# Kernel tuning notes

Hardware: AMD Instinct MI355X
Metric: run time of the kernel (lower is better)

The kernel has to match this reference:

```python
import jax, jax.numpy as jnp
import numpy as np
from jax.scipy.special import logsumexp

BN_EPS = 1e-5
K_CLUSTERS = 32


def _conv1x1(x, W, b):
    # x: [B, Cin, N], W: [Cout, Cin] -> [B, Cout, N]
    return jnp.einsum('oc,bcn->bon', W, x) + b[None, :, None]


def _bn3(x, g, b):
    # BatchNorm1d (training mode, batch stats) over [B, C, N]
    m = x.mean(axis=(0, 2), keepdims=True)
    v = x.var(axis=(0, 2), keepdims=True)
    return g[None, :, None] * (x - m) / jnp.sqrt(v + BN_EPS) + b[None, :, None]


def _bn2(x, g, b):
    # BatchNorm1d (training mode, batch stats) over [B, C]
    m = x.mean(axis=0)
    v = x.var(axis=0)
    return g * (x - m) / jnp.sqrt(v + BN_EPS) + b


def _conv_proj(x, w1, b1, g1, t1, w2, b2, g2, t2, w3, b3):
    h = jax.nn.relu(_bn3(_conv1x1(x, w1, b1), g1, t1))
    h = jax.nn.relu(_bn3(_conv1x1(h, w2, b2), g2, t2))
    return _conv1x1(h, w3, b3)


def _mlp_proj(x, w1, b1, g1, t1, w2, b2, g2, t2, w3, b3):
    h = jax.nn.relu(_bn2(x @ w1.T + b1, g1, t1))
    h = jax.nn.relu(_bn2(h @ w2.T + b2, g2, t2))
    return h @ w3.T + b3


def _normalize(x, axis):
    n = jnp.linalg.norm(x, axis=axis, keepdims=True)
    return x / jnp.maximum(n, 1e-12)


def _sinkhorn_gamma(cost, p, q, eps=1e-3, thresh=1e-3, max_iter=25):
    # log-domain Sinkhorn with early stopping, mirrors the torch loop exactly
    logp = jnp.log(p + 1e-8)
    logq = jnp.log(q + 1e-8)

    def Kf(u, v):
        return (-cost + u[..., :, None] + v[..., None, :]) / eps

    def body(st):
        i, u, v, _ = st
        u0, v0 = u, v
        u = eps * (logp - logsumexp(Kf(u, v), axis=-1)) + u
        v = eps * (logq - logsumexp(Kf(u, v), axis=-2)) + v
        d = jnp.mean(jnp.sum(jnp.abs(u - u0), -1) + jnp.sum(jnp.abs(v - v0), -1))
        return i + 1, u, v, d

    def cond(st):
        return (st[0] < max_iter) & (st[3] >= thresh)

    init = (0, jnp.zeros_like(p), jnp.zeros_like(q), jnp.asarray(jnp.inf, cost.dtype))
    _, u, v, _ = jax.lax.while_loop(cond, body, init)
    return jnp.exp(Kf(u, v))


def _forward(features,
             cw1, cb1, cg1, ct1, cw2, cb2, cg2, ct2, cw3, cb3,
             pw1, pb1, pg1, pt1, pw2, pb2, pg2, pt2, pw3, pb3,
             mw1, mb1, mg1, mt1, mw2, mb2, mg2, mt2, mw3, mb3):
    bs, dim, num = features.shape
    Kc = K_CLUSTERS

    log_score = _conv_proj(features, cw1, cb1, cg1, ct1, cw2, cb2, cg2, ct2, cw3, cb3)  # [B,K,N]
    score = jax.nn.softmax(log_score, axis=1)
    pi = jax.lax.stop_gradient(jnp.clip(score.sum(-1), 1e-4)[:, None, :])  # [B,1,K]
    vlad = jnp.einsum('bkn,bdn->bdk', score, features) / pi  # [B,D,K] (mu == vlad)

    # no-grad Sinkhorn assignment (xyz is None branch, dst='fe')
    nf = _normalize(jax.lax.stop_gradient(features), axis=1)
    nmu = _normalize(jax.lax.stop_gradient(vlad), axis=1)
    cost = jax.lax.stop_gradient(2.0 - 2.0 * jnp.einsum('bdn,bdm->bnm', nf, nmu))  # [B,N,K]
    p = jnp.full((bs, num), 1.0 / num, dtype=features.dtype)
    q = jnp.full((bs, Kc), 1.0 / Kc, dtype=features.dtype)
    gamma = _sinkhorn_gamma(cost, p, q, eps=1e-3, thresh=1e-3, max_iter=25)
    assign = jax.lax.stop_gradient(num * jnp.swapaxes(gamma, -1, -2))  # [B,K,N]

    loss = -jnp.mean(jnp.sum(assign * jax.nn.log_softmax(log_score, axis=1), axis=1))

    c_vlad = _mlp_proj(jnp.max(vlad, axis=-1),
                       mw1, mb1, mg1, mt1, mw2, mb2, mg2, mt2, mw3, mb3)  # [B,proj]
    vlad_out = _conv_proj(vlad, pw1, pb1, pg1, pt1, pw2, pb2, pg2, pt2, pw3, pb3)  # [B,proj,K]
    return loss, vlad_out, c_vlad


def setup_inputs() -> dict:
    B, D, N, Kc, H, P = 8, 1024, 4096, 32, 512, 128
    key = jax.random.key(0)
    ks = jax.random.split(key, 16)

    def w(k, out_c, in_c):
        return (jax.random.normal(k, (out_c, in_c), jnp.float32) / np.sqrt(in_c)).astype(jnp.float32)

    d = {'features': jax.random.normal(ks[0], (B, D, N), jnp.float32)}
    # score conv head: D -> H -> H -> Kc  (hidden = dim // 2 = 512)
    d.update(cw1=w(ks[1], H, D), cb1=jnp.zeros(H), cg1=jnp.ones(H), ct1=jnp.zeros(H),
             cw2=w(ks[2], H, H), cb2=jnp.zeros(H), cg2=jnp.ones(H), ct2=jnp.zeros(H),
             cw3=w(ks[3], Kc, H), cb3=jnp.zeros(Kc))
    # projector conv: D -> 512 -> 512 -> P
    d.update(pw1=w(ks[4], H, D), pb1=jnp.zeros(H), pg1=jnp.ones(H), pt1=jnp.zeros(H),
             pw2=w(ks[5], H, H), pb2=jnp.zeros(H), pg2=jnp.ones(H), pt2=jnp.zeros(H),
             pw3=w(ks[6], P, H), pb3=jnp.zeros(P))
    # predictor MLP: D -> 512 -> 512 -> P
    d.update(mw1=w(ks[7], H, D), mb1=jnp.zeros(H), mg1=jnp.ones(H), mt1=jnp.zeros(H),
             mw2=w(ks[8], H, H), mb2=jnp.zeros(H), mg2=jnp.ones(H), mt2=jnp.zeros(H),
             mw3=w(ks[9], P, H), mb3=jnp.zeros(P))
    return d


def reference(features,
              cw1, cb1, cg1, ct1, cw2, cb2, cg2, ct2, cw3, cb3,
              pw1, pb1, pg1, pt1, pw2, pb2, pg2, pt2, pw3, pb3,
              mw1, mb1, mg1, mt1, mw2, mb2, mg2, mt2, mw3, mb3):
    return _forward(features,
                    cw1, cb1, cg1, ct1, cw2, cb2, cg2, ct2, cw3, cb3,
                    pw1, pb1, pg1, pt1, pw2, pb2, pg2, pt2, pw3, pb3,
                    mw1, mb1, mg1, mt1, mw2, mb2, mg2, mt2, mw3, mb3)
```

## Files before the change

### kernel.cpp

```cpp
#include <hip/hip_runtime.h>
#include <cmath>

#define BB 8
#define DD 1024
#define NP 4096
#define KC 32
#define HH 512
#define PP 128
#define NJB 16
#define BN_EPS 1e-5f
#define NSLOT 32

typedef unsigned short u16;
typedef unsigned long long u64;
typedef short s16x8 __attribute__((ext_vector_type(8)));
typedef float f32x4 __attribute__((ext_vector_type(4)));

__device__ __forceinline__ float waveReduceSum(float v) {
#pragma unroll
  for (int o = 32; o > 0; o >>= 1) v += __shfl_down(v, o, 64);
  return v;
}

__device__ __forceinline__ void split3(float y, short& h, short& m, short& l) {
  unsigned uy = __float_as_uint(y);
  h = (short)(uy >> 16);
  float r1 = y - __uint_as_float(uy & 0xFFFF0000u);
  unsigned um = __float_as_uint(r1);
  m = (short)(um >> 16);
  float r2 = r1 - __uint_as_float(um & 0xFFFF0000u);
  l = (short)(__float_as_uint(r2) >> 16);
}

__global__ __launch_bounds__(256) void convW3_all(
    const float* __restrict__ W1, u16* __restrict__ h1, u16* __restrict__ m1, u16* __restrict__ l1,
    const float* __restrict__ W2, u16* __restrict__ h2, u16* __restrict__ m2, u16* __restrict__ l2,
    const float* __restrict__ W3, u16* __restrict__ h3, u16* __restrict__ m3, u16* __restrict__ l3,
    float* __restrict__ zbuf) {
  int z = blockIdx.z;
  if (z == 2 && blockIdx.x >= 1) {
    int id = (blockIdx.x - 1) * 32 + blockIdx.y;
#pragma unroll
    for (int k2 = 0; k2 < 3; k2++) {
      int idx = k2 * 24576 + id * 256 + (int)threadIdx.x;
      if (idx < 69632) zbuf[idx] = 0.f;
    }
    return;
  }
  const float* W; u16 *hb, *mb, *lb; int K, BM, MTt, KCH;
  if (z == 0)      { W = W1; hb = h1; mb = m1; lb = l1; K = 1024; BM = 128; MTt = 4; KCH = 32; }
  else if (z == 1) { W = W2; hb = h2; mb = m2; lb = l2; K = 512;  BM = 128; MTt = 4; KCH = 16; }
  else             { W = W3; hb = h3; mb = m3; lb = l3; K = 512;  BM = 32;  MTt = 1; KCH = 16; }
  int mt = blockIdx.x, kc = blockIdx.y;
  if (mt >= MTt || kc >= KCH) return;
  const int AU = BM * 4;
  for (int u = threadIdx.x; u < AU; u += 256) {
    int q = u / BM, m = u % BM;
    const float* wp = W + (size_t)(mt * BM + m) * K + kc * 32 + q * 8;
    s16x8 hv, mv, lv;
#pragma unroll
    for (int j = 0; j < 8; j++) {
      short h, mm, l; split3(wp[j], h, mm, l);
      hv[j] = h; mv[j] = mm; lv[j] = l;
    }
    size_t ob = ((size_t)(mt * KCH + kc)) * (size_t)(BM * 32) + (size_t)u * 8;
    *(s16x8*)(hb + ob) = hv;
    *(s16x8*)(mb + ob) = mv;
    *(s16x8*)(lb + ob) = lv;
  }
}

template<int BM, int MBLK, int MT, int NT, int WM, bool BNRELU, bool ACCST, bool SMAX>
__global__ __launch_bounds__(256) void gemm_mfma3(
    const u16* __restrict__ wh, const u16* __restrict__ wmid, const u16* __restrict__ wl,
    const float* __restrict__ bias, const float* __restrict__ X,
    const float* __restrict__ insum, const float* __restrict__ insq,
    const float* __restrict__ bng, const float* __restrict__ bnb, float cnt,
    float* __restrict__ Y, int K, int M,
    float* __restrict__ gsum, float* __restrict__ gsq,
    float* __restrict__ score, float* __restrict__ lse, float* __restrict__ piraw) {
  __shared__ s16x8 AhS[BM * 4], AmS[BM * 4], AlS[BM * 4];
  __shared__ s16x8 BhS[512], BmS[512], BlS[512];
  __shared__ float scS[512], shS[512];
  const int KCH = K / 32;
  const int tid = threadIdx.x;
  const int bz = blockIdx.z;
  int bid = blockIdx.x;
  int xs = bid & 7, rr = bid >> 3;
  int m_idx = rr % MBLK;
  int n_idx = xs + 8 * (rr / MBLK);

  const int w = tid >> 6, l = tid & 63, q = l >> 4, col = l & 15;
  const int wm = (WM == 1) ? 0 : (w >> 1);
  const int wn = (WM == 1) ? w : (w & 1);
  constexpr int NA = (BM * 4 + 255) / 256;

  if (BNRELU) {
    for (int c0 = tid; c0 < K; c0 += 256) {
      float s = 0.f, q2 = 0.f;
      for (int sl = 0; sl < NSLOT; sl++) { s += insum[sl * 512 + c0]; q2 += insq[sl * 512 + c0]; }
      float mean = s / cnt;
      float var = q2 / cnt - mean * mean;
      float sc = bng[c0] / sqrtf(var + BN_EPS);
      scS[c0] = sc; shS[c0] = bnb[c0] - mean * sc;
    }
    __syncthreads();
  }

  f32x4 acc[MT][NT];
#pragma unroll
  for (int i = 0; i < MT; i++)
#pragma unroll
    for (int j = 0; j < NT; j++) { acc[i][j][0] = 0.f; acc[i][j][1] = 0.f; acc[i][j][2] = 0.f; acc[i][j][3] = 0.f; }

// ... 231 lines not shown
      float ra[8], rb[2];
#pragma unroll
      for (int i = 0; i < 8; i++) ra[i] = As[kk][ty * 8 + i];
      rb[0] = Bs[kk][tx * 2]; rb[1] = Bs[kk][tx * 2 + 1];
#pragma unroll
      for (int i = 0; i < 8; i++) { acc[i][0] = fmaf(ra[i], rb[0], acc[i][0]); acc[i][1] = fmaf(ra[i], rb[1], acc[i][1]); }
    }
    __syncthreads();
  }
#pragma unroll
  for (int i = 0; i < 8; i++)
#pragma unroll
    for (int j = 0; j < 2; j++)
      atomicAdd(&vlad[((size_t)b * DD + d0 + ty * 8 + i) * KC + tx * 2 + j], acc[i][j]);
}

__global__ __launch_bounds__(256) void cost_accum(
    const float* __restrict__ feat, const float* __restrict__ vlad,
    const float* __restrict__ piraw, float* __restrict__ costd,
    float* __restrict__ nfsq, float* __restrict__ nmusq, float* __restrict__ gmax) {
  int sp = blockIdx.x, nt = blockIdx.y, b = blockIdx.z;
  int n0 = nt * 128;
  int d_start = sp * (DD / 4);
  __shared__ float As[32][132];
  __shared__ float Bs[32][36];
  __shared__ float nfs[128];
  __shared__ float piS[KC];
  __shared__ float nms[KC];
  int tid = threadIdx.x;
  int tx = tid % 16;
  int ty = tid / 16;
  if (tid < KC) { piS[tid] = fmaxf(piraw[b * KC + tid], 1e-4f); nms[tid] = 0.f; }
  __syncthreads();
  float acc[8][2] = {};
  float sq = 0.f, nm_local = 0.f;
  const float* fb = feat + (size_t)b * DD * NP;
  const float* vb = vlad + (size_t)b * DD * KC;
  for (int dc = 0; dc < DD / 4; dc += 32) {
    int dd0 = d_start + dc;
    for (int i = tid; i < 32 * 128; i += 256) {
      int r = i >> 7, c = i & 127;
      float v = fb[(size_t)(dd0 + r) * NP + n0 + c];
      As[r][c] = v;
      sq = fmaf(v, v, sq);
    }
    for (int i = tid; i < 32 * 32; i += 256) {
      int r = i >> 5, c = i & 31;
      float v = vb[(size_t)(dd0 + r) * KC + c] / piS[c];
      Bs[r][c] = v;
      if (nt == 0) nm_local = fmaf(v, v, nm_local);
    }
    __syncthreads();
    if (nt == 0 && tid < 32) {
      float gm = -1e30f;
#pragma unroll
      for (int c = 0; c < KC; c++) gm = fmaxf(gm, Bs[tid][c]);
      gmax[(size_t)b * DD + dd0 + tid] = gm;
    }
#pragma unroll 4
    for (int kk = 0; kk < 32; kk++) {
      float ra[8], rb[2];
#pragma unroll
      for (int i = 0; i < 8; i++) ra[i] = As[kk][ty * 8 + i];
      rb[0] = Bs[kk][tx * 2]; rb[1] = Bs[kk][tx * 2 + 1];
#pragma unroll
      for (int i = 0; i < 8; i++) { acc[i][0] = fmaf(ra[i], rb[0], acc[i][0]); acc[i][1] = fmaf(ra[i], rb[1], acc[i][1]); }
    }
    __syncthreads();
  }
#pragma unroll
  for (int i = 0; i < 8; i++)
#pragma unroll
    for (int j = 0; j < 2; j++)
      atomicAdd(&costd[((size_t)b * NP + n0 + ty * 8 + i) * KC + tx * 2 + j], acc[i][j]);
  if (tid < 128) nfs[tid] = 0.f;
  __syncthreads();
  atomicAdd(&nfs[tid & 127], sq);
  if (nt == 0) atomicAdd(&nms[tid & 31], nm_local);
  __syncthreads();
  if (tid < 128) atomicAdd(&nfsq[(size_t)b * NP + n0 + tid], nfs[tid]);
  if (nt == 0 && tid < KC) atomicAdd(&nmusq[b * KC + tid], nms[tid]);
}

__global__ __launch_bounds__(256) void sinkhorn_all(
    const float* __restrict__ costd, const float* __restrict__ nfsq,
    const float* __restrict__ nmusq, u64* __restrict__ G,
    const float* __restrict__ LSm, const float* __restrict__ lseArr,
    float* __restrict__ out0, unsigned* __restrict__ flags,
    float logp, float logq) {
  const float EPS = 1e-3f, IEPS = 1000.f;
  int b = blockIdx.x / NJB, j = blockIdx.x % NJB;
  int tid = threadIdx.x;
  int n = j * 256 + tid;
  __shared__ float vsh[KC];
  __shared__ float nmS[KC];
  __shared__ float vals[256][33];
  __shared__ float red[KC][9];
  __shared__ float bmS[KC];
  __shared__ float redL[4];

  if (tid < KC) nmS[tid] = fmaxf(sqrtf(nmusq[b * KC + tid]), 1e-12f);
  __syncthreads();

  float c[KC];
  {
    const float* dp = costd + ((size_t)b * NP + n) * KC;
    float nf = fmaxf(sqrtf(nfsq[(size_t)b * NP + n]), 1e-12f);
#pragma unroll
    for (int k = 0; k < KC; k++) c[k] = 2.f - 2.f * dp[k] / (nf * nmS[k]);
  }

  const int kk = tid & 31, seg = tid >> 5;
  const int r0 = seg * 32;
  float u = 0.f;

  for (int t = 1; t <= 25; t++) {
    if (t > 1) {
      if (tid < NJB) {
        const unsigned* fp = flags + ((size_t)(t - 2) * BB + b) * NJB;
        while (__hip_atomic_load(&fp[tid], __ATOMIC_RELAXED, __HIP_MEMORY_SCOPE_AGENT) == 0u)
          __builtin_amdgcn_s_sleep(1);
      }
      __syncthreads();
    }
    if (tid < KC) {
      float v = 0.f;
      if (t > 1) {
        const u64* Gp = G + (((size_t)(t - 2) * BB + b) * NJB) * KC;
        float gm[NJB], gs[NJB];
#pragma unroll
        for (int jj = 0; jj < NJB; jj++) {
          u64 raw = __hip_atomic_load(&Gp[jj * KC + tid], __ATOMIC_RELAXED, __HIP_MEMORY_SCOPE_AGENT);
          gm[jj] = __uint_as_float((unsigned)raw);
          gs[jj] = __uint_as_float((unsigned)(raw >> 32));
        }
        float m = -1e30f;
#pragma unroll
        for (int jj = 0; jj < NJB; jj++) m = fmaxf(m, gm[jj]);
        float s = 0.f;
#pragma unroll
        for (int jj = 0; jj < NJB; jj++) s += gs[jj] * expf(gm[jj] - m);
        v = EPS * logq - EPS * (m + logf(s));
      }
      vsh[tid] = v;
    }
    __syncthreads();
    float m = -1e30f;
#pragma unroll
    for (int k = 0; k < KC; k++) m = fmaxf(m, vsh[k] - c[k]);
    float s = 0.f;
#pragma unroll
    for (int k = 0; k < KC; k++) s += expf((vsh[k] - c[k] - m) * IEPS);
    u = EPS * logp - m - EPS * logf(s);
#pragma unroll
    for (int k = 0; k < KC; k++) vals[tid][k] = (u - c[k]) * IEPS;
    __syncthreads();
    {
      float lm = -1e30f;
      for (int r = 0; r < 32; r++) lm = fmaxf(lm, vals[r0 + r][kk]);
      red[kk][seg] = lm;
    }
    __syncthreads();
    if (tid < KC) {
      float bm = red[tid][0];
      for (int i2 = 1; i2 < 8; i2++) bm = fmaxf(bm, red[tid][i2]);
      bmS[tid] = bm;
    }
    __syncthreads();
    {
      float bm = bmS[kk];
      float ls = 0.f;
      for (int r = 0; r < 32; r++) ls += expf(vals[r0 + r][kk] - bm);
      red[kk][seg] = ls;
    }
    __syncthreads();
    if (tid < KC) {
      float s8 = 0.f;
      for (int i2 = 0; i2 < 8; i2++) s8 += red[tid][i2];
      u64 raw = (u64)__float_as_uint(bmS[tid]) | ((u64)__float_as_uint(s8) << 32);
      u64* Gp = G + (((size_t)(t - 1) * BB + b) * NJB + j) * KC + tid;
      __hip_atomic_store(Gp, raw, __ATOMIC_RELAXED, __HIP_MEMORY_SCOPE_AGENT);
    }
    __syncthreads();
    if (tid == 0) {
      unsigned* fl = flags + ((size_t)(t - 1) * BB + b) * NJB + j;
      __hip_atomic_store(fl, 1u, __ATOMIC_RELAXED, __HIP_MEMORY_SCOPE_AGENT);
    }
  }

  if (tid < NJB) {
    const unsigned* fp = flags + ((size_t)24 * BB + b) * NJB;
    while (__hip_atomic_load(&fp[tid], __ATOMIC_RELAXED, __HIP_MEMORY_SCOPE_AGENT) == 0u)
      __builtin_amdgcn_s_sleep(1);
  }
  __syncthreads();
  __shared__ float v25S[KC];
  if (tid < KC) {
    const u64* Gp = G + (((size_t)24 * BB + b) * NJB) * KC;
    float gm[NJB], gs[NJB];
#pragma unroll
    for (int jj = 0; jj < NJB; jj++) {
      u64 raw = __hip_atomic_load(&Gp[jj * KC + tid], __ATOMIC_RELAXED, __HIP_MEMORY_SCOPE_AGENT);
      gm[jj] = __uint_as_float((unsigned)raw);
      gs[jj] = __uint_as_float((unsigned)(raw >> 32));
    }
    float m = -1e30f;
#pragma unroll
    for (int jj = 0; jj < NJB; jj++) m = fmaxf(m, gm[jj]);
    float s = 0.f;
#pragma unroll
    for (int jj = 0; jj < NJB; jj++) s += gs[jj] * expf(gm[jj] - m);
    v25S[tid] = EPS * logq - EPS * (m + logf(s));
  }
  __syncthreads();
  float lsev = lseArr[(size_t)b * NP + n];
  float part = 0.f;
#pragma unroll
  for (int k = 0; k < KC; k++) {
    float gamma = expf((u + v25S[k] - c[k]) * IEPS);
    float logsm = LSm[((size_t)b * KC + k) * NP + n] - lsev;
    part += gamma * logsm;
  }
  part *= (float)NP;
  int lane = tid & 63, wid = tid >> 6;
  part = waveReduceSum(part);
  if (lane == 0) redL[wid] = part;
  __syncthreads();
  if (tid == 0) {
    float tt = redL[0] + redL[1] + redL[2] + redL[3];
    atomicAdd(out0, -tt / (float)(BB * NP));
  }
}

template<int BM, int BN, int BK, int TM, int TN, bool BNRELU, bool ACCST, bool PDIV>
__global__ __launch_bounds__(256) void gemm_conv(
    const float* __restrict__ W, const float* __restrict__ bias,
    const float* __restrict__ X, float* __restrict__ Y,
    const float* __restrict__ pidiv,
    const float* __restrict__ insum, const float* __restrict__ insq,
    const float* __restrict__ bng, const float* __restrict__ bnb, float cnt,
    float* __restrict__ gsum, float* __restrict__ gsq,
    int M, int K, int N) {
  __shared__ float As[BK][BM + 4];
  __shared__ float Xs[BK][BN + 4];
  __shared__ float scS[512], shS[512];
  __shared__ float piS[BN + 4];
  const int b = blockIdx.z;
  const int m0 = blockIdx.y * BM;
  const int n0 = blockIdx.x * BN;
  const int tid = threadIdx.x;
  const int tx = tid % (BN / TN);
  const int ty = tid / (BN / TN);
  if (PDIV) {
    if (tid < N) piS[tid] = fmaxf(pidiv[b * N + tid], 1e-4f);
  }
  if (BNRELU) {
    for (int c0 = tid; c0 < K; c0 += 256) {
      float mean = insum[c0] / cnt;
      float var = insq[c0] / cnt - mean * mean;
      float sc = bng[c0] / sqrtf(var + BN_EPS);
      scS[c0] = sc; shS[c0] = bnb[c0] - mean * sc;
    }
  }
  if (PDIV || BNRELU) __syncthreads();
  const float* Xb = X + (size_t)b * K * N;
  float acc[TM][TN];
#pragma unroll
  for (int i = 0; i < TM; i++)
#pragma unroll
    for (int j = 0; j < TN; j++) acc[i][j] = 0.f;

  for (int k0 = 0; k0 < K; k0 += BK) {
    for (int i = tid; i < BM * BK; i += 256) {
      int r = i / BK, c = i % BK;
      As[c][r] = W[(size_t)(m0 + r) * K + k0 + c];
    }
    for (int i = tid; i < BK * BN; i += 256) {
      int r = i / BN, c = i % BN;
      float x = Xb[(size_t)(k0 + r) * N + n0 + c];
      if (PDIV) x /= piS[n0 + c];
      if (BNRELU) x = fmaxf(fmaf(x, scS[k0 + r], shS[k0 + r]), 0.f);
      Xs[r][c] = x;
    }
    __syncthreads();
#pragma unroll 4
    for (int kk = 0; kk < BK; kk++) {
      float ra[TM], rb[TN];
#pragma unroll
      for (int i = 0; i < TM; i++) ra[i] = As[kk][ty * TM + i];
#pragma unroll
      for (int j = 0; j < TN; j++) rb[j] = Xs[kk][tx * TN + j];
#pragma unroll
      for (int i = 0; i < TM; i++)
#pragma unroll
        for (int j = 0; j < TN; j++) acc[i][j] = fmaf(ra[i], rb[j], acc[i][j]);
    }
    __syncthreads();
  }
  float* red = (float*)As;
  if (ACCST) {
    if (tid < 2 * BM) red[tid] = 0.f;
    __syncthreads();
  }
#pragma unroll
  for (int i = 0; i < TM; i++) {
    int ml = ty * TM + i;
    float bm = bias[m0 + ml];
    float ys = 0.f, yq = 0.f;
#pragma unroll
    for (int j = 0; j < TN; j++) {
      float y = acc[i][j] + bm;
      Y[((size_t)b * M + m0 + ml) * N + n0 + tx * TN + j] = y;
      ys += y; yq = fmaf(y, y, yq);
    }
    if (ACCST) {
      atomicAdd(&red[ml * 2], ys);
      atomicAdd(&red[ml * 2 + 1], yq);
    }
  }
  if (ACCST) {
    __syncthreads();
    if (tid < BM) {
      atomicAdd(&gsum[m0 + tid], red[tid * 2]);
      atomicAdd(&gsq[m0 + tid], red[tid * 2 + 1]);
    }
  }
}

template<bool BNRELU, bool ACCST>
__global__ __launch_bounds__(256) void mlp_gemm(
    const float* __restrict__ W, const float* __restrict__ bias,
    const float* __restrict__ in, float* __restrict__ out,
    const float* __restrict__ insum, const float* __restrict__ insq,
    const float* __restrict__ g, const float* __restrict__ beta,
    float* __restrict__ gsum, float* __restrict__ gsq, int M, int K) {
  __shared__ float scS[512], shS[512];
  int tid = threadIdx.x;
  if (BNRELU) {
    for (int c0 = tid; c0 < K; c0 += 256) {
      float mean = insum[c0] * 0.125f;
      float var = insq[c0] * 0.125f - mean * mean;
      float sc = g[c0] / sqrtf(var + BN_EPS);
      scS[c0] = sc; shS[c0] = beta[c0] - mean * sc;
    }
    __syncthreads();
  }
  int gw = (blockIdx.x * 256 + tid) >> 6;
  int lane = tid & 63;
  int s = gw / M, jj = gw % M;
  const float4* ip = (const float4*)(in + (size_t)s * K);
  const float4* wp = (const float4*)(W + (size_t)jj * K);
  float acc = 0.f;
  for (int c4 = lane; c4 < (K >> 2); c4 += 64) {
    float4 x = ip[c4];
    float4 w = wp[c4];
    if (BNRELU) {
      int cb = c4 * 4;
      x.x = fmaxf(fmaf(x.x, scS[cb + 0], shS[cb + 0]), 0.f);
      x.y = fmaxf(fmaf(x.y, scS[cb + 1], shS[cb + 1]), 0.f);
      x.z = fmaxf(fmaf(x.z, scS[cb + 2], shS[cb + 2]), 0.f);
      x.w = fmaxf(fmaf(x.w, scS[cb + 3], shS[cb + 3]), 0.f);
    }
    acc += x.x * w.x + x.y * w.y + x.z * w.z + x.w * w.w;
  }
  acc = waveReduceSum(acc);
  if (lane == 0) {
    float y = acc + bias[jj];
    out[gw] = y;
    if (ACCST) { atomicAdd(&gsum[jj], y); atomicAdd(&gsq[jj], y * y); }
  }
}

extern "C" void kernel_launch(void* const* d_in, const int* in_sizes, int n_in,
                              void* d_out, int out_size, void* d_ws, size_t ws_size,
                              hipStream_t stream) {
  const float* feat = (const float*)d_in[0];
  const float* cw1 = (const float*)d_in[1];  const float* cb1 = (const float*)d_in[2];
  const float* cg1 = (const float*)d_in[3];  const float* ct1 = (const float*)d_in[4];
  const float* cw2 = (const float*)d_in[5];  const float* cb2 = (const float*)d_in[6];
  const float* cg2 = (const float*)d_in[7];  const float* ct2 = (const float*)d_in[8];
  const float* cw3 = (const float*)d_in[9];  const float* cb3 = (const float*)d_in[10];
  const float* pw1 = (const float*)d_in[11]; const float* pb1 = (const float*)d_in[12];
  const float* pg1 = (const float*)d_in[13]; const float* pt1 = (const float*)d_in[14];
  const float* pw2 = (const float*)d_in[15]; const float* pb2 = (const float*)d_in[16];
  const float* pg2 = (const float*)d_in[17]; const float* pt2 = (const float*)d_in[18];
  const float* pw3 = (const float*)d_in[19]; const float* pb3 = (const float*)d_in[20];
  const float* mw1 = (const float*)d_in[21]; const float* mb1 = (const float*)d_in[22];
  const float* mg1 = (const float*)d_in[23]; const float* mt1 = (const float*)d_in[24];
  const float* mw2 = (const float*)d_in[25]; const float* mb2 = (const float*)d_in[26];
  const float* mg2 = (const float*)d_in[27]; const float* mt2 = (const float*)d_in[28];
  const float* mw3 = (const float*)d_in[29]; const float* mb3 = (const float*)d_in[30];
  float* out = (float*)d_out;

  char* p = (char*)d_ws;
  size_t off = 0;
  auto alloc = [&](size_t bytes) { char* r = p + off; off = (off + bytes + 255) & ~(size_t)255; return r; };
  float* Y1 = (float*)alloc(67108864);
  float* Y2 = (float*)alloc(67108864);
  u16* W1H = (u16*)alloc(1048576); u16* W1M = (u16*)alloc(1048576); u16* W1L = (u16*)alloc(1048576);
  u16* W2H = (u16*)alloc(524288);  u16* W2M = (u16*)alloc(524288);  u16* W2L = (u16*)alloc(524288);
  u16* W3H = (u16*)alloc(32768);   u16* W3M = (u16*)alloc(32768);   u16* W3L = (u16*)alloc(32768);
  float* BNACC = (float*)alloc(278528);
  float* GS1 = BNACC + 0;      float* GQ1 = BNACC + 16384;
  float* GS2 = BNACC + 32768;  float* GQ2 = BNACC + 49152;
  float* MSS1 = BNACC + 65536; float* MSQ1 = BNACC + 66048;
  float* MSS2 = BNACC + 66560; float* MSQ2 = BNACC + 67072;
  float* PS1 = BNACC + 67584;  float* PQ1 = BNACC + 68096;
  float* PS2 = BNACC + 68608;  float* PQ2 = BNACC + 69120;
  char* q = (char*)Y1;
  size_t qoff = 0;
  auto qalloc = [&](size_t bytes) { char* r = q + qoff; qoff = (qoff + bytes + 255) & ~(size_t)255; return r; };
  float* LSC  = (float*)qalloc(4194304);
  float* SCRB = (float*)qalloc(4194304);
  float* LSE  = (float*)qalloc(131072);
  u64*   GBUF = (u64*)qalloc(819200);
  float* GMAX = (float*)qalloc(32768);
  float* MH1  = (float*)qalloc(16384);
  float* MH2  = (float*)qalloc(16384);
  float* T1   = (float*)qalloc(524288);
  float* T2   = (float*)qalloc(524288);
  const size_t MS_BYTES = 1024 + 1048576 + 4194304 + 131072 + 1024 + 16384;
  char* MS = qalloc(MS_BYTES);
  float* PIRAW = (float*)MS;
  float* VLAD  = (float*)(MS + 1024);
  float* COSTD = (float*)(MS + 1024 + 1048576);
  float* NFSQ  = (float*)(MS + 1024 + 1048576 + 4194304);
  float* NMUSQ = (float*)(MS + 1024 + 1048576 + 4194304 + 131072);
  unsigned* FLG = (unsigned*)(MS + 1024 + 1048576 + 4194304 + 131072 + 1024);

  hipMemsetAsync(d_out, 0, sizeof(float), stream);

  float logp = logf(1.0f / NP + 1e-8f);
  float logq = logf(1.0f / KC + 1e-8f);
  const float CNT_BN = (float)(BB * NP);
  const float CNT_PJ = (float)(BB * KC);
  dim3 blk(256);

  convW3_all<<<dim3(4, 32, 3), blk, 0, stream>>>(
      cw1, W1H, W1M, W1L, cw2, W2H, W2M, W2L, cw3, W3H, W3M, W3L, BNACC);

  gemm_mfma3<128, 4, 4, 4, 2, false, true, false><<<dim3(128, 1, 8), blk, 0, stream>>>(
      W1H, W1M, W1L, cb1, feat, nullptr, nullptr, nullptr, nullptr, 0.f,
      Y1, 1024, 512, GS1, GQ1, nullptr, nullptr, nullptr);
  gemm_mfma3<128, 4, 4, 4, 2, true, true, false><<<dim3(128, 1, 8), blk, 0, stream>>>(
      W2H, W2M, W2L, cb2, Y1, GS1, GQ1, cg1, ct1, CNT_BN,
      Y2, 512, 512, GS2, GQ2, nullptr, nullptr, nullptr);
  hipMemsetAsync(MS, 0, MS_BYTES, stream);
  gemm_mfma3<32, 1, 2, 2, 1, true, false, true><<<dim3(32, 1, 8), blk, 0, stream>>>(
      W3H, W3M, W3L, cb3, Y2, GS2, GQ2, cg2, ct2, CNT_BN,
      LSC, 512, 32, nullptr, nullptr, SCRB, LSE, PIRAW);

  vlad_accum<<<dim3(8, DD / 128, BB), blk, 0, stream>>>(feat, SCRB, VLAD);

  cost_accum<<<dim3(4, NP / 128, BB), blk, 0, stream>>>(
      feat, VLAD, PIRAW, COSTD, NFSQ, NMUSQ, GMAX);

  sinkhorn_all<<<dim3(BB * NJB), blk, 0, stream>>>(
      COSTD, NFSQ, NMUSQ, GBUF, LSC, LSE, out, FLG, logp, logq);

  mlp_gemm<false, true><<<dim3(BB * HH / 4), blk, 0, stream>>>(
      mw1, mb1, GMAX, MH1, nullptr, nullptr, nullptr, nullptr, MSS1, MSQ1, HH, DD);
  mlp_gemm<true, true><<<dim3(BB * HH / 4), blk, 0, stream>>>(
      mw2, mb2, MH1, MH2, MSS1, MSQ1, mg1, mt1, MSS2, MSQ2, HH, HH);
  mlp_gemm<true, false><<<dim3(BB * PP / 4), blk, 0, stream>>>(
      mw3, mb3, MH2, out + 1 + BB * PP * KC, MSS2, MSQ2, mg2, mt2, nullptr, nullptr, PP, HH);

  gemm_conv<64, 32, 16, 4, 2, false, true, true><<<dim3(1, HH / 64, BB), blk, 0, stream>>>(
      pw1, pb1, VLAD, T1, PIRAW, nullptr, nullptr, nullptr, nullptr, 0.f, PS1, PQ1, HH, DD, KC);
  gemm_conv<64, 32, 16, 4, 2, true, true, false><<<dim3(1, HH / 64, BB), blk, 0, stream>>>(
      pw2, pb2, T1, T2, nullptr, PS1, PQ1, pg1, pt1, CNT_PJ, PS2, PQ2, HH, HH, KC);
  gemm_conv<64, 32, 16, 4, 2, true, false, false><<<dim3(1, PP / 64, BB), blk, 0, stream>>>(
      pw3, pb3, T2, out + 1, nullptr, PS2, PQ2, pg2, pt2, CNT_PJ, nullptr, nullptr, PP, HH, KC);
}
```

Measured before the change: 1.149 ms.

## Fuse sinkhorn, MLP predictor and conv projector into one persistent tail kernel

Merges the Sinkhorn kernel, three MLP GEMM launches and three projector conv GEMM launches into a single 208-block kernel. Blocks are partitioned by role, so the MLP and projector chains run alongside the Sinkhorn iterations instead of after them. Inter-layer BatchNorm dependencies are handled with software grid barriers built on flag spinning in global memory. This removes six kernel launches and the serialization of independent work. The risks are deadlock if not all 208 blocks are co-resident, and the MLP phase now runs on only 16 blocks, which lowers its parallelism.

```diff
diff --git a/kernel.cpp b/kernel.cpp
--- a/kernel.cpp
+++ b/kernel.cpp
@@ -10,6 +10,10 @@
 #define NJB 16
 #define BN_EPS 1e-5f
 #define NSLOT 32
+#define FOFF_M1 3200
+#define FOFF_M2 3216
+#define FOFF_P1 3232
+#define FOFF_P2 3296
 
 typedef unsigned short u16;
 typedef unsigned long long u64;
@@ -30,6 +34,18 @@
   m = (short)(um >> 16);
   float r2 = r1 - __uint_as_float(um & 0xFFFF0000u);
   l = (short)(__float_as_uint(r2) >> 16);
+}
+
+__device__ void shadowBar(unsigned* flg, int nb, int myid) {
+  __threadfence();
+  __syncthreads();
+  if (threadIdx.x == 0)
+    __hip_atomic_store(&flg[myid], 1u, __ATOMIC_RELAXED, __HIP_MEMORY_SCOPE_AGENT);
+  if ((int)threadIdx.x < nb)
+    while (__hip_atomic_load(&flg[threadIdx.x], __ATOMIC_RELAXED, __HIP_MEMORY_SCOPE_AGENT) == 0u)
+      __builtin_amdgcn_s_sleep(2);
+  __syncthreads();
+  __threadfence();
 }
 
 __global__ __launch_bounds__(256) void convW3_all(
@@ -427,178 +443,19 @@
   if (nt == 0 && tid < KC) atomicAdd(&nmusq[b * KC + tid], nms[tid]);
 }
 
-__global__ __launch_bounds__(256) void sinkhorn_all(
-    const float* __restrict__ costd, const float* __restrict__ nfsq,
-    const float* __restrict__ nmusq, u64* __restrict__ G,
-    const float* __restrict__ LSm, const float* __restrict__ lseArr,
-    float* __restrict__ out0, unsigned* __restrict__ flags,
-    float logp, float logq) {
-  const float EPS = 1e-3f, IEPS = 1000.f;
-  int b = blockIdx.x / NJB, j = blockIdx.x % NJB;
-  int tid = threadIdx.x;
-  int n = j * 256 + tid;
-  __shared__ float vsh[KC];
-  __shared__ float nmS[KC];
-  __shared__ float vals[256][33];
-  __shared__ float red[KC][9];
-  __shared__ float bmS[KC];
-  __shared__ float redL[4];
-
-  if (tid < KC) nmS[tid] = fmaxf(sqrtf(nmusq[b * KC + tid]), 1e-12f);
-  __syncthreads();
-
-  float c[KC];
-  {
-    const float* dp = costd + ((size_t)b * NP + n) * KC;
-    float nf = fmaxf(sqrtf(nfsq[(size_t)b * NP + n]), 1e-12f);
-#pragma unroll
-    for (int k = 0; k < KC; k++) c[k] = 2.f - 2.f * dp[k] / (nf * nmS[k]);
-  }
-
-  const int kk = tid & 31, seg = tid >> 5;
-  const int r0 = seg * 32;
-  float u = 0.f;
-
-  for (int t = 1; t <= 25; t++) {
-    if (t > 1) {
-      if (tid < NJB) {
-        const unsigned* fp = flags + ((size_t)(t - 2) * BB + b) * NJB;
-        while (__hip_atomic_load(&fp[tid], __ATOMIC_RELAXED, __HIP_MEMORY_SCOPE_AGENT) == 0u)
-          __builtin_amdgcn_s_sleep(1);
-      }
-      __syncthreads();
-    }
-    if (tid < KC) {
-      float v = 0.f;
-      if (t > 1) {
-        const u64* Gp = G + (((size_t)(t - 2) * BB + b) * NJB) * KC;
-        float gm[NJB], gs[NJB];
-#pragma unroll
-        for (int jj = 0; jj < NJB; jj++) {
-          u64 raw = __hip_atomic_load(&Gp[jj * KC + tid], __ATOMIC_RELAXED, __HIP_MEMORY_SCOPE_AGENT);
-          gm[jj] = __uint_as_float((unsigned)raw);
-          gs[jj] = __uint_as_float((unsigned)(raw >> 32));
-        }
-        float m = -1e30f;
-#pragma unroll
-        for (int jj = 0; jj < NJB; jj++) m = fmaxf(m, gm[jj]);
-        float s = 0.f;
-#pragma unroll
-        for (int jj = 0; jj < NJB; jj++) s += gs[jj] * expf(gm[jj] - m);
-        v = EPS * logq - EPS * (m + logf(s));
-      }
-      vsh[tid] = v;
-    }
-    __syncthreads();
-    float m = -1e30f;
-#pragma unroll
-    for (int k = 0; k < KC; k++) m = fmaxf(m, vsh[k] - c[k]);
-    float s = 0.f;
-#pragma unroll
-    for (int k = 0; k < KC; k++) s += expf((vsh[k] - c[k] - m) * IEPS);
-    u = EPS * logp - m - EPS * logf(s);
-#pragma unroll
-    for (int k = 0; k < KC; k++) vals[tid][k] = (u - c[k]) * IEPS;
-    __syncthreads();
-    {
-      float lm = -1e30f;
-      for (int r = 0; r < 32; r++) lm = fmaxf(lm, vals[r0 + r][kk]);
-      red[kk][seg] = lm;
-    }
-    __syncthreads();
-    if (tid < KC) {
-      float bm = red[tid][0];
-      for (int i2 = 1; i2 < 8; i2++) bm = fmaxf(bm, red[tid][i2]);
-      bmS[tid] = bm;
-    }
-    __syncthreads();
-    {
-      float bm = bmS[kk];
-      float ls = 0.f;
-      for (int r = 0; r < 32; r++) ls += expf(vals[r0 + r][kk] - bm);
-      red[kk][seg] = ls;
-    }
-    __syncthreads();
-    if (tid < KC) {
-      float s8 = 0.f;
-      for (int i2 = 0; i2 < 8; i2++) s8 += red[tid][i2];
-      u64 raw = (u64)__float_as_uint(bmS[tid]) | ((u64)__float_as_uint(s8) << 32);
-      u64* Gp = G + (((size_t)(t - 1) * BB + b) * NJB + j) * KC + tid;
-      __hip_atomic_store(Gp, raw, __ATOMIC_RELAXED, __HIP_MEMORY_SCOPE_AGENT);
-    }
-    __syncthreads();
-    if (tid == 0) {
-      unsigned* fl = flags + ((size_t)(t - 1) * BB + b) * NJB + j;
-      __hip_atomic_store(fl, 1u, __ATOMIC_RELAXED, __HIP_MEMORY_SCOPE_AGENT);
-    }
-  }
-
-  if (tid < NJB) {
-    const unsigned* fp = flags + ((size_t)24 * BB + b) * NJB;
-    while (__hip_atomic_load(&fp[tid], __ATOMIC_RELAXED, __HIP_MEMORY_SCOPE_AGENT) == 0u)
-      __builtin_amdgcn_s_sleep(1);
-  }
-  __syncthreads();
-  __shared__ float v25S[KC];
-  if (tid < KC) {
-    const u64* Gp = G + (((size_t)24 * BB + b) * NJB) * KC;
-    float gm[NJB], gs[NJB];
-#pragma unroll
-    for (int jj = 0; jj < NJB; jj++) {
-      u64 raw = __hip_atomic_load(&Gp[jj * KC + tid], __ATOMIC_RELAXED, __HIP_MEMORY_SCOPE_AGENT);
-      gm[jj] = __uint_as_float((unsigned)raw);
-      gs[jj] = __uint_as_float((unsigned)(raw >> 32));
-    }
-    float m = -1e30f;
-#pragma unroll
-    for (int jj = 0; jj < NJB; jj++) m = fmaxf(m, gm[jj]);
-    float s = 0.f;
-#pragma unroll
-    for (int jj = 0; jj < NJB; jj++) s += gs[jj] * expf(gm[jj] - m);
-    v25S[tid] = EPS * logq - EPS * (m + logf(s));
-  }
-  __syncthreads();
-  float lsev = lseArr[(size_t)b * NP + n];
-  float part = 0.f;
-#pragma unroll
-  for (int k = 0; k < KC; k++) {
-    float gamma = expf((u + v25S[k] - c[k]) * IEPS);
-    float logsm = LSm[((size_t)b * KC + k) * NP + n] - lsev;
-    part += gamma * logsm;
-  }
-  part *= (float)NP;
-  int lane = tid & 63, wid = tid >> 6;
-  part = waveReduceSum(part);
-  if (lane == 0) redL[wid] = part;
-  __syncthreads();
-  if (tid == 0) {
-    float tt = redL[0] + redL[1] + redL[2] + redL[3];
-    atomicAdd(out0, -tt / (float)(BB * NP));
-  }
-}
-
-template<int BM, int BN, int BK, int TM, int TN, bool BNRELU, bool ACCST, bool PDIV>
-__global__ __launch_bounds__(256) void gemm_conv(
+template<bool BNRELU, bool ACCST, bool PDIV>
+__device__ void proj_layer(float (*As)[68], float (*Xs)[36], float* scS, float* shS, float* piS,
     const float* __restrict__ W, const float* __restrict__ bias,
     const float* __restrict__ X, float* __restrict__ Y,
     const float* __restrict__ pidiv,
     const float* __restrict__ insum, const float* __restrict__ insq,
     const float* __restrict__ bng, const float* __restrict__ bnb, float cnt,
     float* __restrict__ gsum, float* __restrict__ gsq,
-    int M, int K, int N) {
-  __shared__ float As[BK][BM + 4];
-  __shared__ float Xs[BK][BN + 4];
-  __shared__ float scS[512], shS[512];
-  __shared__ float piS[BN + 4];
-  const int b = blockIdx.z;
-  const int m0 = blockIdx.y * BM;
-  const int n0 = blockIdx.x * BN;
+    int M, int K, int b, int m0) {
   const int tid = threadIdx.x;
-  const int tx = tid % (BN / TN);
-  const int ty = tid / (BN / TN);
-  if (PDIV) {
-    if (tid < N) piS[tid] = fmaxf(pidiv[b * N + tid], 1e-4f);
-  }
+  const int tx = tid % 16;
+  const int ty = tid / 16;
+  if (PDIV && tid < KC) piS[tid] = fmaxf(pidiv[b * KC + tid], 1e-4f);
   if (BNRELU) {
     for (int c0 = tid; c0 < K; c0 += 256) {
       float mean = insum[c0] / cnt;
@@ -607,55 +464,47 @@
       scS[c0] = sc; shS[c0] = bnb[c0] - mean * sc;
     }
   }
-  if (PDIV || BNRELU) __syncthreads();
-  const float* Xb = X + (size_t)b * K * N;
-  float acc[TM][TN];
-#pragma unroll
-  for (int i = 0; i < TM; i++)
-#pragma unroll
-    for (int j = 0; j < TN; j++) acc[i][j] = 0.f;
-
-  for (int k0 = 0; k0 < K; k0 += BK) {
-    for (int i = tid; i < BM * BK; i += 256) {
-      int r = i / BK, c = i % BK;
+  __syncthreads();
+  const float* Xb = X + (size_t)b * K * KC;
+  float acc[4][2] = {};
+  for (int k0 = 0; k0 < K; k0 += 16) {
+    for (int i = tid; i < 64 * 16; i += 256) {
+      int r = i / 16, c = i % 16;
       As[c][r] = W[(size_t)(m0 + r) * K + k0 + c];
     }
-    for (int i = tid; i < BK * BN; i += 256) {
-      int r = i / BN, c = i % BN;
-      float x = Xb[(size_t)(k0 + r) * N + n0 + c];
-      if (PDIV) x /= piS[n0 + c];
+    for (int i = tid; i < 16 * 32; i += 256) {
+      int r = i / 32, c = i % 32;
+      float x = Xb[(size_t)(k0 + r) * KC + c];
+      if (PDIV) x /= piS[c];
       if (BNRELU) x = fmaxf(fmaf(x, scS[k0 + r], shS[k0 + r]), 0.f);
       Xs[r][c] = x;
     }
     __syncthreads();
 #pragma unroll 4
-    for (int kk = 0; kk < BK; kk++) {
-      float ra[TM], rb[TN];
-#pragma unroll
-      for (int i = 0; i < TM; i++) ra[i] = As[kk][ty * TM + i];
-#pragma unroll
-      for (int j = 0; j < TN; j++) rb[j] = Xs[kk][tx * TN + j];
-#pragma unroll
-      for (int i = 0; i < TM; i++)
-#pragma unroll
-        for (int j = 0; j < TN; j++) acc[i][j] = fmaf(ra[i], rb[j], acc[i][j]);
+    for (int kk = 0; kk < 16; kk++) {
+      float ra[4], rb[2];
+#pragma unroll
+      for (int i = 0; i < 4; i++) ra[i] = As[kk][ty * 4 + i];
+      rb[0] = Xs[kk][tx * 2]; rb[1] = Xs[kk][tx * 2 + 1];
+#pragma unroll
+      for (int i = 0; i < 4; i++) { acc[i][0] = fmaf(ra[i], rb[0], acc[i][0]); acc[i][1] = fmaf(ra[i], rb[1], acc[i][1]); }
     }
     __syncthreads();
   }
   float* red = (float*)As;
   if (ACCST) {
-    if (tid < 2 * BM) red[tid] = 0.f;
-    __syncthreads();
-  }
-#pragma unroll
-  for (int i = 0; i < TM; i++) {
-    int ml = ty * TM + i;
+    if (tid < 128) red[tid] = 0.f;
+    __syncthreads();
+  }
+#pragma unroll
+  for (int i = 0; i < 4; i++) {
+    int ml = ty * 4 + i;
     float bm = bias[m0 + ml];
     float ys = 0.f, yq = 0.f;
 #pragma unroll
-    for (int j = 0; j < TN; j++) {
+    for (int j = 0; j < 2; j++) {
       float y = acc[i][j] + bm;
-      Y[((size_t)b * M + m0 + ml) * N + n0 + tx * TN + j] = y;
+      Y[((size_t)b * M + m0 + ml) * KC + tx * 2 + j] = y;
       ys += y; yq = fmaf(y, y, yq);
     }
     if (ACCST) {
@@ -665,54 +514,282 @@
   }
   if (ACCST) {
     __syncthreads();
-    if (tid < BM) {
+    if (tid < 64) {
       atomicAdd(&gsum[m0 + tid], red[tid * 2]);
-      atomicAdd(&gsq[m0 + tid], red[tid * 2 + 1]);
-    }
-  }
-}
-
-template<bool BNRELU, bool ACCST>
-__global__ __launch_bounds__(256) void mlp_gemm(
-    const float* __restrict__ W, const float* __restrict__ bias,
-    const float* __restrict__ in, float* __restrict__ out,
-    const float* __restrict__ insum, const float* __restrict__ insq,
-    const float* __restrict__ g, const float* __restrict__ beta,
-    float* __restrict__ gsum, float* __restrict__ gsq, int M, int K) {
-  __shared__ float scS[512], shS[512];
-  int tid = threadIdx.x;
-  if (BNRELU) {
-    for (int c0 = tid; c0 < K; c0 += 256) {
-      float mean = insum[c0] * 0.125f;
-      float var = insq[c0] * 0.125f - mean * mean;
-      float sc = g[c0] / sqrtf(var + BN_EPS);
-      scS[c0] = sc; shS[c0] = beta[c0] - mean * sc;
-    }
-    __syncthreads();
-  }
-  int gw = (blockIdx.x * 256 + tid) >> 6;
-  int lane = tid & 63;
-  int s = gw / M, jj = gw % M;
-  const float4* ip = (const float4*)(in + (size_t)s * K);
-  const float4* wp = (const float4*)(W + (size_t)jj * K);
-  float acc = 0.f;
-  for (int c4 = lane; c4 < (K >> 2); c4 += 64) {
-    float4 x = ip[c4];
-    float4 w = wp[c4];
-    if (BNRELU) {
-      int cb = c4 * 4;
-      x.x = fmaxf(fmaf(x.x, scS[cb + 0], shS[cb + 0]), 0.f);
-      x.y = fmaxf(fmaf(x.y, scS[cb + 1], shS[cb + 1]), 0.f);
-      x.z = fmaxf(fmaf(x.z, scS[cb + 2], shS[cb + 2]), 0.f);
-      x.w = fmaxf(fmaf(x.w, scS[cb + 3], shS[cb + 3]), 0.f);
-    }
-    acc += x.x * w.x + x.y * w.y + x.z * w.z + x.w * w.w;
-  }
-  acc = waveReduceSum(acc);
-  if (lane == 0) {
-    float y = acc + bias[jj];
-    out[gw] = y;
-    if (ACCST) { atomicAdd(&gsum[jj], y); atomicAdd(&gsq[jj], y * y); }
+      atomicAdd(&gsq [m0 + tid], red[tid * 2 + 1]);
+    }
+  }
+}
+
+__global__ __launch_bounds__(256) void tail_all(
+    const float* __restrict__ costd, const float* __restrict__ nfsq,
+    const float* __restrict__ nmusq, u64* __restrict__ G,
+    const float* __restrict__ LSm, const float* __restrict__ lseArr,
+    float* __restrict__ out0, unsigned* __restrict__ flags,
+    float logp, float logq,
+    const float* __restrict__ mw1, const float* __restrict__ mb1,
+    const float* __restrict__ mg1, const float* __restrict__ mt1,
+    const float* __restrict__ mw2, const float* __restrict__ mb2,
+    const float* __restrict__ mg2, const float* __restrict__ mt2,
+    const float* __restrict__ mw3, const float* __restrict__ mb3,
+    const float* __restrict__ gmax, float* __restrict__ mh1, float* __restrict__ mh2,
+    float* __restrict__ outm,
+    float* __restrict__ mss1, float* __restrict__ msq1,
+    float* __restrict__ mss2, float* __restrict__ msq2,
+    const float* __restrict__ pw1, const float* __restrict__ pb1,
+    const float* __restrict__ pg1, const float* __restrict__ pt1,
+    const float* __restrict__ pw2, const float* __restrict__ pb2,
+    const float* __restrict__ pg2, const float* __restrict__ pt2,
+    const float* __restrict__ pw3, const float* __restrict__ pb3,
+    const float* __restrict__ vlad, const float* __restrict__ piraw,
+    float* __restrict__ t1, float* __restrict__ t2, float* __restrict__ outp,
+    float* __restrict__ ps1, float* __restrict__ pq1,
+    float* __restrict__ ps2, float* __restrict__ pq2) {
+  __shared__ float smemF[9216];
+  const int bid = blockIdx.x;
+  const int tid = threadIdx.x;
+
+  if (bid < 128) {
+    const float EPS = 1e-3f, IEPS = 1000.f;
+    float* vsh  = smemF;
+    float* nmS  = smemF + 32;
+    float* bmS  = smemF + 64;
+    float* redL = smemF + 96;
+    float* v25S = smemF + 100;
+    float (*vals)[33] = (float(*)[33])(smemF + 160);
+    float (*red)[9]   = (float(*)[9])(smemF + 160 + 8448);
+    int b = bid / NJB, j = bid % NJB;
+    int n = j * 256 + tid;
+
+    if (tid < KC) nmS[tid] = fmaxf(sqrtf(nmusq[b * KC + tid]), 1e-12f);
+    __syncthreads();
+
+    float c[KC];
+    {
+      const float* dp = costd + ((size_t)b * NP + n) * KC;
+      float nf = fmaxf(sqrtf(nfsq[(size_t)b * NP + n]), 1e-12f);
+#pragma unroll
+      for (int k = 0; k < KC; k++) c[k] = 2.f - 2.f * dp[k] / (nf * nmS[k]);
+    }
+
+    const int kk = tid & 31, seg = tid >> 5;
+    const int r0 = seg * 32;
+    float u = 0.f;
+
+    for (int t = 1; t <= 25; t++) {
+      if (t > 1) {
+        if (tid < NJB) {
+          const unsigned* fp = flags + ((size_t)(t - 2) * BB + b) * NJB;
+          while (__hip_atomic_load(&fp[tid], __ATOMIC_RELAXED, __HIP_MEMORY_SCOPE_AGENT) == 0u)
+            __builtin_amdgcn_s_sleep(1);
+        }
+        __syncthreads();
+      }
+      if (tid < KC) {
+        float v = 0.f;
+        if (t > 1) {
+          const u64* Gp = G + (((size_t)(t - 2) * BB + b) * NJB) * KC;
+          float gm[NJB], gs[NJB];
+#pragma unroll
+          for (int jj = 0; jj < NJB; jj++) {
+            u64 raw = __hip_atomic_load(&Gp[jj * KC + tid], __ATOMIC_RELAXED, __HIP_MEMORY_SCOPE_AGENT);
+            gm[jj] = __uint_as_float((unsigned)raw);
+            gs[jj] = __uint_as_float((unsigned)(raw >> 32));
+          }
+          float m = -1e30f;
+#pragma unroll
+          for (int jj = 0; jj < NJB; jj++) m = fmaxf(m, gm[jj]);
+          float s = 0.f;
+#pragma unroll
+          for (int jj = 0; jj < NJB; jj++) s += gs[jj] * expf(gm[jj] - m);
+          v = EPS * logq - EPS * (m + logf(s));
+        }
+        vsh[tid] = v;
+      }
+      __syncthreads();
+      float m = -1e30f;
+#pragma unroll
+      for (int k = 0; k < KC; k++) m = fmaxf(m, vsh[k] - c[k]);
+      float s = 0.f;
+#pragma unroll
+      for (int k = 0; k < KC; k++) s += expf((vsh[k] - c[k] - m) * IEPS);
+      u = EPS * logp - m - EPS * logf(s);
+#pragma unroll
+      for (int k = 0; k < KC; k++) vals[tid][k] = (u - c[k]) * IEPS;
+      __syncthreads();
+      {
+        float lm = -1e30f;
+        for (int r = 0; r < 32; r++) lm = fmaxf(lm, vals[r0 + r][kk]);
+        red[kk][seg] = lm;
+      }
+      __syncthreads();
+      if (tid < KC) {
+        float bm = red[tid][0];
+        for (int i2 = 1; i2 < 8; i2++) bm = fmaxf(bm, red[tid][i2]);
+        bmS[tid] = bm;
+      }
+      __syncthreads();
+      {
+        float bm = bmS[kk];
+        float ls = 0.f;
+        for (int r = 0; r < 32; r++) ls += expf(vals[r0 + r][kk] - bm);
+        red[kk][seg] = ls;
+      }
+      __syncthreads();
+      if (tid < KC) {
+        float s8 = 0.f;
+        for (int i2 = 0; i2 < 8; i2++) s8 += red[tid][i2];
+        u64 raw = (u64)__float_as_uint(bmS[tid]) | ((u64)__float_as_uint(s8) << 32);
+        u64* Gp = G + (((size_t)(t - 1) * BB + b) * NJB + j) * KC + tid;
+        __hip_atomic_store(Gp, raw, __ATOMIC_RELAXED, __HIP_MEMORY_SCOPE_AGENT);
+      }
+      __syncthreads();
+      if (tid == 0) {
+        unsigned* fl = flags + ((size_t)(t - 1) * BB + b) * NJB + j;
+        __hip_atomic_store(fl, 1u, __ATOMIC_RELAXED, __HIP_MEMORY_SCOPE_AGENT);
+      }
+    }
+
+    if (tid < NJB) {
+      const unsigned* fp = flags + ((size_t)24 * BB + b) * NJB;
+      while (__hip_atomic_load(&fp[tid], __ATOMIC_RELAXED, __HIP_MEMORY_SCOPE_AGENT) == 0u)
+        __builtin_amdgcn_s_sleep(1);
+    }
+    __syncthreads();
+    if (tid < KC) {
+      const u64* Gp = G + (((size_t)24 * BB + b) * NJB) * KC;
+      float gm[NJB], gs[NJB];
+#pragma unroll
+      for (int jj = 0; jj < NJB; jj++) {
+        u64 raw = __hip_atomic_load(&Gp[jj * KC + tid], __ATOMIC_RELAXED, __HIP_MEMORY_SCOPE_AGENT);
+        gm[jj] = __uint_as_float((unsigned)raw);
+        gs[jj] = __uint_as_float((unsigned)(raw >> 32));
+      }
+      float m = -1e30f;
+#pragma unroll
+      for (int jj = 0; jj < NJB; jj++) m = fmaxf(m, gm[jj]);
+      float s = 0.f;
+#pragma unroll
+      for (int jj = 0; jj < NJB; jj++) s += gs[jj] * expf(gm[jj] - m);
+      v25S[tid] = EPS * logq - EPS * (m + logf(s));
+    }
+    __syncthreads();
+    float lsev = lseArr[(size_t)b * NP + n];
+    float part = 0.f;
+#pragma unroll
+    for (int k = 0; k < KC; k++) {
+      float gamma = expf((u + v25S[k] - c[k]) * IEPS);
+      float logsm = LSm[((size_t)b * KC + k) * NP + n] - lsev;
+      part += gamma * logsm;
+    }
+    part *= (float)NP;
+    int lane = tid & 63, wid = tid >> 6;
+    part = waveReduceSum(part);
+    if (lane == 0) redL[wid] = part;
+    __syncthreads();
+    if (tid == 0) {
+      float tt = redL[0] + redL[1] + redL[2] + redL[3];
+      atomicAdd(out0, -tt / (float)(BB * NP));
+    }
+  } else if (bid < 144) {
+    float* scS = smemF;
+    float* shS = smemF + 512;
+    int mid = bid - 128;
+    int wv = mid * 4 + (tid >> 6);
+    int lane = tid & 63;
+    for (int t = 0; t < 64; t++) {
+      int idx = wv * 64 + t;
+      int s = idx >> 9, jj = idx & 511;
+      const float4* ip = (const float4*)(gmax + (size_t)s * DD);
+      const float4* wp = (const float4*)(mw1 + (size_t)jj * DD);
+      float acc = 0.f;
+      for (int c4 = lane; c4 < DD / 4; c4 += 64) {
+        float4 x = ip[c4]; float4 w = wp[c4];
+        acc += x.x * w.x + x.y * w.y + x.z * w.z + x.w * w.w;
+      }
+      acc = waveReduceSum(acc);
+      if (lane == 0) {
+        float y = acc + mb1[jj];
+        mh1[idx] = y;
+        atomicAdd(&mss1[jj], y); atomicAdd(&msq1[jj], y * y);
+      }
+    }
+    shadowBar(flags + FOFF_M1, 16, mid);
+    for (int c0 = tid; c0 < HH; c0 += 256) {
+      float mean = mss1[c0] * 0.125f;
+      float var = msq1[c0] * 0.125f - mean * mean;
+      float sc = mg1[c0] / sqrtf(var + BN_EPS);
+      scS[c0] = sc; shS[c0] = mt1[c0] - mean * sc;
+    }
+    __syncthreads();
+    for (int t = 0; t < 64; t++) {
+      int idx = wv * 64 + t;
+      int s = idx >> 9, jj = idx & 511;
+      const float4* ip = (const float4*)(mh1 + (size_t)s * HH);
+      const float4* wp = (const float4*)(mw2 + (size_t)jj * HH);
+      float acc = 0.f;
+      for (int c4 = lane; c4 < HH / 4; c4 += 64) {
+        float4 x = ip[c4]; float4 w = wp[c4];
+        int cb = c4 * 4;
+        x.x = fmaxf(fmaf(x.x, scS[cb + 0], shS[cb + 0]), 0.f);
+        x.y = fmaxf(fmaf(x.y, scS[cb + 1], shS[cb + 1]), 0.f);
+        x.z = fmaxf(fmaf(x.z, scS[cb + 2], shS[cb + 2]), 0.f);
+        x.w = fmaxf(fmaf(x.w, scS[cb + 3], shS[cb + 3]), 0.f);
+        acc += x.x * w.x + x.y * w.y + x.z * w.z + x.w * w.w;
+      }
+      acc = waveReduceSum(acc);
+      if (lane == 0) {
+        float y = acc + mb2[jj];
+        mh2[idx] = y;
+        atomicAdd(&mss2[jj], y); atomicAdd(&msq2[jj], y * y);
+      }
+    }
+    shadowBar(flags + FOFF_M2, 16, mid);
+    for (int c0 = tid; c0 < HH; c0 += 256) {
+      float mean = mss2[c0] * 0.125f;
+      float var = msq2[c0] * 0.125f - mean * mean;
+      float sc = mg2[c0] / sqrtf(var + BN_EPS);
+      scS[c0] = sc; shS[c0] = mt2[c0] - mean * sc;
+    }
+    __syncthreads();
+    for (int t = 0; t < 16; t++) {
+      int idx = wv * 16 + t;
+      int s = idx >> 7, jj = idx & 127;
+      const float4* ip = (const float4*)(mh2 + (size_t)s * HH);
+      const float4* wp = (const float4*)(mw3 + (size_t)jj * HH);
+      float acc = 0.f;
+      for (int c4 = lane; c4 < HH / 4; c4 += 64) {
+        float4 x = ip[c4]; float4 w = wp[c4];
+        int cb = c4 * 4;
+        x.x = fmaxf(fmaf(x.x, scS[cb + 0], shS[cb + 0]), 0.f);
+        x.y = fmaxf(fmaf(x.y, scS[cb + 1], shS[cb + 1]), 0.f);
+        x.z = fmaxf(fmaf(x.z, scS[cb + 2], shS[cb + 2]), 0.f);
+        x.w = fmaxf(fmaf(x.w, scS[cb + 3], shS[cb + 3]), 0.f);
+        acc += x.x * w.x + x.y * w.y + x.z * w.z + x.w * w.w;
+      }
+      acc = waveReduceSum(acc);
+      if (lane == 0) outm[idx] = acc + mb3[jj];
+    }
+  } else {
+    float (*As)[68] = (float(*)[68])smemF;
+    float (*Xs)[36] = (float(*)[36])(smemF + 1088);
+    float* scS = smemF + 1664;
+    float* shS = smemF + 2176;
+    float* piS = smemF + 2688;
+    int pid = bid - 144;
+    int b = pid >> 3, mt = pid & 7;
+    proj_layer<false, true, true>(As, Xs, scS, shS, piS,
+        pw1, pb1, vlad, t1, piraw, nullptr, nullptr, nullptr, nullptr, 0.f,
+        ps1, pq1, HH, DD, b, mt * 64);
+    shadowBar(flags + FOFF_P1, 64, pid);
+    proj_layer<true, true, false>(As, Xs, scS, shS, piS,
+        pw2, pb2, t1, t2, nullptr, ps1, pq1, pg1, pt1, (float)(BB * KC),
+        ps2, pq2, HH, HH, b, mt * 64);
+    shadowBar(flags + FOFF_P2, 64, pid);
+    if (mt < 2)
+      proj_layer<true, false, false>(As, Xs, scS, shS, piS,
+          pw3, pb3, t2, outp, nullptr, ps2, pq2, pg2, pt2, (float)(BB * KC),
+          nullptr, nullptr, PP, HH, b, mt * 64);
   }
 }
 
@@ -778,7 +855,6 @@
   float logp = logf(1.0f / NP + 1e-8f);
   float logq = logf(1.0f / KC + 1e-8f);
   const float CNT_BN = (float)(BB * NP);
-  const float CNT_PJ = (float)(BB * KC);
   dim3 blk(256);
 
   convW3_all<<<dim3(4, 32, 3), blk, 0, stream>>>(
@@ -800,20 +876,10 @@
   cost_accum<<<dim3(4, NP / 128, BB), blk, 0, stream>>>(
       feat, VLAD, PIRAW, COSTD, NFSQ, NMUSQ, GMAX);
 
-  sinkhorn_all<<<dim3(BB * NJB), blk, 0, stream>>>(
-      COSTD, NFSQ, NMUSQ, GBUF, LSC, LSE, out, FLG, logp, logq);
-
-  mlp_gemm<false, true><<<dim3(BB * HH / 4), blk, 0, stream>>>(
-      mw1, mb1, GMAX, MH1, nullptr, nullptr, nullptr, nullptr, MSS1, MSQ1, HH, DD);
-  mlp_gemm<true, true><<<dim3(BB * HH / 4), blk, 0, stream>>>(
-      mw2, mb2, MH1, MH2, MSS1, MSQ1, mg1, mt1, MSS2, MSQ2, HH, HH);
-  mlp_gemm<true, false><<<dim3(BB * PP / 4), blk, 0, stream>>>(
-      mw3, mb3, MH2, out + 1 + BB * PP * KC, MSS2, MSQ2, mg2, mt2, nullptr, nullptr, PP, HH);
-
-  gemm_conv<64, 32, 16, 4, 2, false, true, true><<<dim3(1, HH / 64, BB), blk, 0, stream>>>(
-      pw1, pb1, VLAD, T1, PIRAW, nullptr, nullptr, nullptr, nullptr, 0.f, PS1, PQ1, HH, DD, KC);
-  gemm_conv<64, 32, 16, 4, 2, true, true, false><<<dim3(1, HH / 64, BB), blk, 0, stream>>>(
-      pw2, pb2, T1, T2, nullptr, PS1, PQ1, pg1, pt1, CNT_PJ, PS2, PQ2, HH, HH, KC);
-  gemm_conv<64, 32, 16, 4, 2, true, false, false><<<dim3(1, PP / 64, BB), blk, 0, stream>>>(
-      pw3, pb3, T2, out + 1, nullptr, PS2, PQ2, pg2, pt2, CNT_PJ, nullptr, nullptr, PP, HH, KC);
-}
+  tail_all<<<dim3(208), blk, 0, stream>>>(
+      COSTD, NFSQ, NMUSQ, GBUF, LSC, LSE, out, FLG, logp, logq,
+      mw1, mb1, mg1, mt1, mw2, mb2, mg2, mt2, mw3, mb3,
+      GMAX, MH1, MH2, out + 1 + BB * PP * KC, MSS1, MSQ1, MSS2, MSQ2,
+      pw1, pb1, pg1, pt1, pw2, pb2, pg2, pt2, pw3, pb3,
+      VLAD, PIRAW, T1, T2, out + 1, PS1, PQ1, PS2, PQ2);
+}
```

Result: faster. 1.005 ms (-12.5%).
